# Kernel optimization log

Hardware: AMD Instinct MI355X
Metric: run time of the kernel (lower is better)

## Reference

```python
import jax, jax.numpy as jnp
import numpy as np
from jax import lax

QK_K = 256          # elements per Q6_K super-block
TYPE_SIZE = 210     # bytes per Q6_K super-block (128 ql + 64 qh + 16 scales + 2 d)
OUT_F = 14336
IN_F = 4096


def setup_inputs() -> dict:
    key = jax.random.key(0)
    kx, kb = jax.random.split(key)
    x = jax.random.normal(kx, (16, 1, IN_F), dtype=jnp.float32)
    bias = jax.random.normal(kb, (OUT_F,), dtype=jnp.float32) * 0.02

    # Build realistic packed Q6_K weight bytes with numpy (bit packing).
    rng = np.random.default_rng(0)
    n_blocks = OUT_F * IN_F // QK_K
    ql = rng.integers(0, 256, (n_blocks, 128), dtype=np.uint8)
    qh = rng.integers(0, 256, (n_blocks, 64), dtype=np.uint8)
    scales = rng.integers(-32, 32, (n_blocks, 16)).astype(np.int8).view(np.uint8)
    d = (rng.standard_normal(n_blocks) * 0.004).astype(np.float16).view(np.uint8).reshape(n_blocks, 2)
    w_q = jnp.asarray(np.concatenate([ql, qh, scales, d], axis=1))  # [n_blocks, 210] uint8
    return {"x": x, "w_q": w_q, "bias": bias}


def _dequant_q6_k(w_q, out_f, in_f):
    # w_q: [n_blocks, 210] uint8 -> [out_f, in_f] float32
    n = w_q.shape[0]
    ql = w_q[:, :128].astype(jnp.int32)
    qh = w_q[:, 128:192].astype(jnp.int32)
    sc = lax.bitcast_convert_type(w_q[:, 192:208], jnp.int8).astype(jnp.float32)  # [n,16]
    d_u16 = w_q[:, 208].astype(jnp.uint16) | (w_q[:, 209].astype(jnp.uint16) << 8)
    d = lax.bitcast_convert_type(d_u16, jnp.float16).astype(jnp.float32)          # [n]
    dl = (d[:, None] * sc).reshape(n, 16, 1)                                      # per-16-elt scale

    shift_l = jnp.array([0, 4], dtype=jnp.int32).reshape(1, 1, 2, 1)
    ql = ((ql.reshape(n, 2, 1, 64) >> shift_l) & 15).reshape(n, 8, 32)
    shift_h = jnp.array([0, 2, 4, 6], dtype=jnp.int32).reshape(1, 1, 4, 1)
    qh = ((qh.reshape(n, 2, 1, 32) >> shift_h) & 3).reshape(n, 8, 32)
    q = (ql | (qh << 4)) - 32                                                     # int in [-32, 31]
    w = dl * q.reshape(n, 16, 16).astype(jnp.float32)
    return w.reshape(out_f, in_f)


def reference(x, w_q, bias):
    in_f = x.shape[-1]
    out_f = bias.shape[0]
    w = _dequant_q6_k(w_q, out_f, in_f)          # [out_f, in_f]
    return jnp.einsum("bsi,oi->bso", x, w) + bias
```

## Files before the change

kernel.cpp:

```cpp
#include <hip/hip_runtime.h>
#include <hip/hip_bf16.h>
#include <hip/hip_fp16.h>
#include <stdint.h>


#define OUT_F 14336
#define IN_F  4096
#define NB    16

using f32x4  = __attribute__((ext_vector_type(4))) float;
using short8 = __attribute__((ext_vector_type(8))) short;

constexpr int ROWS = 64;
constexpr int SBS  = 2;
constexpr int SLOT = 216;
constexpr int ROWSTRIDE = SBS * SLOT + 8;
constexpr int KSPLIT = IN_F / (SBS * 256);

__device__ __forceinline__ float ub(uint32_t v, int i) {
  return (float)((v >> (8 * i)) & 0xffu);
}
__device__ __forceinline__ uint32_t pack_bf16(float lo, float hi) {
  return (__builtin_bit_cast(uint32_t, lo) >> 16) |
         (__builtin_bit_cast(uint32_t, hi) & 0xffff0000u);
}

__global__ __launch_bounds__(256)
void prep_kernel(const float* __restrict__ x, const float* __restrict__ bias,
                 float* __restrict__ out, ushort* __restrict__ xbf, int use_ws)
{
  const int t = blockIdx.x * 256 + threadIdx.x;
  if (t < NB * OUT_F) {
    out[t] = bias[t % OUT_F];
  }
  if (use_ws && t < NB * IN_F) {
    uint32_t u = __builtin_bit_cast(uint32_t, x[t]);
    xbf[t] = (ushort)((u + 0x8000u) >> 16);
  }
}

template<bool USE_WS>
__global__ __launch_bounds__(256, 4)
void q6k_gemm(const int* __restrict__ wq,
              const float* __restrict__ xf,
              const ushort* __restrict__ xbf,
              float* __restrict__ out)
{
  __shared__ uint8_t lds[ROWS * ROWSTRIDE];
  const int tid = threadIdx.x;
  const int bx  = blockIdx.x;
  const int by  = blockIdx.y;
  const int row_base = bx * ROWS;

  ushort* lds16 = (ushort*)lds;
  for (int i = tid; i < ROWS * 105; i += 256) {
    const int r = i / 105;
    const int d = i - r * 105;
    const int4 q4 = *(const int4*)(wq + (size_t)(row_base + r) * 3360 + by * 420 + 4 * d);
    const uint32_t v = (uint32_t)(q4.x & 0xff) | ((uint32_t)(q4.y & 0xff) << 8) |
                       ((uint32_t)(q4.z & 0xff) << 16) | ((uint32_t)q4.w << 24);
    const int b0 = 4 * d, b1 = 4 * d + 2;
    const int sb0 = b0 / 210, sb1 = b1 / 210;
    lds16[(r * ROWSTRIDE + sb0 * SLOT + (b0 - sb0 * 210)) >> 1] = (ushort)v;
    lds16[(r * ROWSTRIDE + sb1 * SLOT + (b1 - sb1 * 210)) >> 1] = (ushort)(v >> 16);
  }
  __syncthreads();

  const int lane = tid & 63;
  const int wv   = tid >> 6;
  const int l15  = lane & 15;
  const int lg   = lane >> 4;
  const int sc_sh = 8 * (lane >> 5);

  f32x4 acc = {0.f, 0.f, 0.f, 0.f};
  const int k_blk = by * (SBS * 256);
  const uint8_t* rowslot = lds + (wv * 16 + l15) * ROWSTRIDE;

  #pragma unroll
  for (int sb = 0; sb < SBS; ++sb) {
    const uint8_t* slot = rowslot + sb * SLOT;
    const uint2 sc01 = *(const uint2*)(slot + 192);
    const uint2 sc23 = *(const uint2*)(slot + 200);
    const float dsup = __half2float(*(const __half*)(slot + 208));
    const int k_sb = k_blk + sb * 256 + 8 * lg;

    #pragma unroll
    for (int m = 0; m < 8; ++m) {
      const uint2 ql = *(const uint2*)(slot + (m >> 2) * 64 + (m & 1) * 32 + 8 * lg);
      const uint2 qh = *(const uint2*)(slot + 128 + (m >> 2) * 32 + 8 * lg);

      const uint32_t scw = (m >> 1) == 0 ? sc01.x : (m >> 1) == 1 ? sc01.y
                         : (m >> 1) == 2 ? sc23.x : sc23.y;
      const int sc = (int)(int8_t)(scw >> (16 * (m & 1) + sc_sh));
      const float dl  = dsup * (float)sc;
      const float mdl = -32.0f * dl;

      const int SL = 4 * ((m >> 1) & 1);
      const int SH = 2 * (m & 3);
      const uint32_t t0 = (ql.x >> SL) & 0x0F0F0F0Fu;
      const uint32_t t1 = (ql.y >> SL) & 0x0F0F0F0Fu;
      const uint32_t h0 = (qh.x >> SH) & 0x03030303u;
      const uint32_t h1 = (qh.y >> SH) & 0x03030303u;
      const uint32_t q0 = t0 | (h0 << 4);
      const uint32_t q1 = t1 | (h1 << 4);

      const float w0 = fmaf(ub(q0, 0), dl, mdl);
      const float w1 = fmaf(ub(q0, 1), dl, mdl);
      const float w2 = fmaf(ub(q0, 2), dl, mdl);
      const float w3 = fmaf(ub(q0, 3), dl, mdl);
      const float w4 = fmaf(ub(q1, 0), dl, mdl);
      const float w5 = fmaf(ub(q1, 1), dl, mdl);
      const float w6 = fmaf(ub(q1, 2), dl, mdl);
      const float w7 = fmaf(ub(q1, 3), dl, mdl);

      union { short8 s; uint32_t u[4]; } bfr;
      bfr.u[0] = pack_bf16(w0, w1);
      bfr.u[1] = pack_bf16(w2, w3);
      bfr.u[2] = pack_bf16(w4, w5);
      bfr.u[3] = pack_bf16(w6, w7);

      short8 afrag;
      if constexpr (USE_WS) {
        afrag = *(const short8*)(xbf + (size_t)l15 * IN_F + k_sb + m * 32);
      } else {
        const float* xp = xf + (size_t)l15 * IN_F + k_sb + m * 32;
        const f32x4 v0 = *(const f32x4*)(xp);
        const f32x4 v1 = *(const f32x4*)(xp + 4);
        union { short8 s; uint32_t u[4]; } av;
        av.u[0] = pack_bf16(v0[0], v0[1]);
        av.u[1] = pack_bf16(v0[2], v0[3]);
        av.u[2] = pack_bf16(v1[0], v1[1]);
        av.u[3] = pack_bf16(v1[2], v1[3]);
        afrag = av.s;
      }

      acc = __builtin_amdgcn_mfma_f32_16x16x32_bf16(afrag, bfr.s, acc, 0, 0, 0);
    }
  }

  const int o = row_base + wv * 16 + l15;
  #pragma unroll
  for (int r = 0; r < 4; ++r) {
    atomicAdd(&out[(size_t)(lg * 4 + r) * OUT_F + o], acc[r]);
  }
}

extern "C" void kernel_launch(void* const* d_in, const int* in_sizes, int n_in,
                              void* d_out, int out_size, void* d_ws, size_t ws_size,
                              hipStream_t stream)
{
  const float* x    = (const float*)d_in[0];
  const int*   wq   = (const int*)d_in[1];
  const float* bias = (const float*)d_in[2];
  float*  out = (float*)d_out;
  ushort* xbf = (ushort*)d_ws;
  const bool use_ws = ws_size >= (size_t)NB * IN_F * 2;

  prep_kernel<<<dim3((NB * OUT_F + 255) / 256), dim3(256), 0, stream>>>(
      x, bias, out, xbf, use_ws ? 1 : 0);

  dim3 grid(OUT_F / ROWS, KSPLIT);
  if (use_ws) {
    q6k_gemm<true><<<grid, dim3(256), 0, stream>>>(wq, x, xbf, out);
  } else {
    q6k_gemm<false><<<grid, dim3(256), 0, stream>>>(wq, x, xbf, out);
  }
}
```

Before: 52.85 us.

## Read Q6_K weight bytes directly from global memory, drop LDS staging

Removes the shared-memory staging pass and block barrier. Each lane now loads its weight bytes straight from global memory, where the weight tensor is stored as one int per byte, and dequantizes them in registers. This cuts the LDS write/read traffic and the __syncthreads. In exchange each lane issues many small strided 8-byte global loads per MFMA step instead of coalesced 16-byte loads, which may hurt memory coalescing and cache efficiency.

Result: slower. 55.87 us (+5.7%).

```diff
diff --git a/kernel.cpp b/kernel.cpp
--- a/kernel.cpp
+++ b/kernel.cpp
@@ -11,15 +11,9 @@
 using f32x4  = __attribute__((ext_vector_type(4))) float;
 using short8 = __attribute__((ext_vector_type(8))) short;
 
-constexpr int ROWS = 64;
-constexpr int SBS  = 2;
-constexpr int SLOT = 216;
-constexpr int ROWSTRIDE = SBS * SLOT + 8;
-constexpr int KSPLIT = IN_F / (SBS * 256);
+constexpr int ROWS   = 64;
+constexpr int KSPLIT = 8;
 
-__device__ __forceinline__ float ub(uint32_t v, int i) {
-  return (float)((v >> (8 * i)) & 0xffu);
-}
 __device__ __forceinline__ uint32_t pack_bf16(float lo, float hi) {
   return (__builtin_bit_cast(uint32_t, lo) >> 16) |
          (__builtin_bit_cast(uint32_t, hi) & 0xffff0000u);
@@ -46,78 +40,58 @@
               const ushort* __restrict__ xbf,
               float* __restrict__ out)
 {
-  __shared__ uint8_t lds[ROWS * ROWSTRIDE];
-  const int tid = threadIdx.x;
-  const int bx  = blockIdx.x;
-  const int by  = blockIdx.y;
-  const int row_base = bx * ROWS;
-
-  ushort* lds16 = (ushort*)lds;
-  for (int i = tid; i < ROWS * 105; i += 256) {
-    const int r = i / 105;
-    const int d = i - r * 105;
-    const int4 q4 = *(const int4*)(wq + (size_t)(row_base + r) * 3360 + by * 420 + 4 * d);
-    const uint32_t v = (uint32_t)(q4.x & 0xff) | ((uint32_t)(q4.y & 0xff) << 8) |
-                       ((uint32_t)(q4.z & 0xff) << 16) | ((uint32_t)q4.w << 24);
-    const int b0 = 4 * d, b1 = 4 * d + 2;
-    const int sb0 = b0 / 210, sb1 = b1 / 210;
-    lds16[(r * ROWSTRIDE + sb0 * SLOT + (b0 - sb0 * 210)) >> 1] = (ushort)v;
-    lds16[(r * ROWSTRIDE + sb1 * SLOT + (b1 - sb1 * 210)) >> 1] = (ushort)(v >> 16);
-  }
-  __syncthreads();
-
+  const int tid  = threadIdx.x;
   const int lane = tid & 63;
   const int wv   = tid >> 6;
   const int l15  = lane & 15;
   const int lg   = lane >> 4;
-  const int sc_sh = 8 * (lane >> 5);
+  const int hb   = lg >> 1;
+  const int by   = blockIdx.y;
+
+  const int row = blockIdx.x * ROWS + wv * 16 + l15;
+  const int* base = wq + (size_t)row * 3360 + by * 420;
+  const int k_blk = by * 512;
 
   f32x4 acc = {0.f, 0.f, 0.f, 0.f};
-  const int k_blk = by * (SBS * 256);
-  const uint8_t* rowslot = lds + (wv * 16 + l15) * ROWSTRIDE;
 
   #pragma unroll
-  for (int sb = 0; sb < SBS; ++sb) {
-    const uint8_t* slot = rowslot + sb * SLOT;
-    const uint2 sc01 = *(const uint2*)(slot + 192);
-    const uint2 sc23 = *(const uint2*)(slot + 200);
-    const float dsup = __half2float(*(const __half*)(slot + 208));
+  for (int sb = 0; sb < 2; ++sb) {
+    const int* sbase = base + sb * 210;
+    const uint2 dd = *(const uint2*)(sbase + 208);
+    const float dsup = __half2float(
+        __builtin_bit_cast(__half, (uint16_t)((dd.x & 0xffu) | ((dd.y & 0xffu) << 8))));
     const int k_sb = k_blk + sb * 256 + 8 * lg;
 
     #pragma unroll
     for (int m = 0; m < 8; ++m) {
-      const uint2 ql = *(const uint2*)(slot + (m >> 2) * 64 + (m & 1) * 32 + 8 * lg);
-      const uint2 qh = *(const uint2*)(slot + 128 + (m >> 2) * 32 + 8 * lg);
+      const int* qlp = sbase + (m >> 2) * 64 + (m & 1) * 32 + 8 * lg;
+      const int* qhp = sbase + 128 + (m >> 2) * 32 + 8 * lg;
+      const uint2 a0 = *(const uint2*)(qlp);
+      const uint2 a1 = *(const uint2*)(qlp + 2);
+      const uint2 a2 = *(const uint2*)(qlp + 4);
+      const uint2 a3 = *(const uint2*)(qlp + 6);
+      const uint2 b0 = *(const uint2*)(qhp);
+      const uint2 b1 = *(const uint2*)(qhp + 2);
+      const uint2 b2 = *(const uint2*)(qhp + 4);
+      const uint2 b3 = *(const uint2*)(qhp + 6);
+      const uint2 scp = *(const uint2*)(sbase + 192 + 2 * m);
 
-      const uint32_t scw = (m >> 1) == 0 ? sc01.x : (m >> 1) == 1 ? sc01.y
-                         : (m >> 1) == 2 ? sc23.x : sc23.y;
-      const int sc = (int)(int8_t)(scw >> (16 * (m & 1) + sc_sh));
+      const int sc = (int)(int8_t)(uint8_t)(hb ? scp.y : scp.x);
       const float dl  = dsup * (float)sc;
       const float mdl = -32.0f * dl;
 
       const int SL = 4 * ((m >> 1) & 1);
       const int SH = 2 * (m & 3);
-      const uint32_t t0 = (ql.x >> SL) & 0x0F0F0F0Fu;
-      const uint32_t t1 = (ql.y >> SL) & 0x0F0F0F0Fu;
-      const uint32_t h0 = (qh.x >> SH) & 0x03030303u;
-      const uint32_t h1 = (qh.y >> SH) & 0x03030303u;
-      const uint32_t q0 = t0 | (h0 << 4);
-      const uint32_t q1 = t1 | (h1 << 4);
-
-      const float w0 = fmaf(ub(q0, 0), dl, mdl);
-      const float w1 = fmaf(ub(q0, 1), dl, mdl);
-      const float w2 = fmaf(ub(q0, 2), dl, mdl);
-      const float w3 = fmaf(ub(q0, 3), dl, mdl);
-      const float w4 = fmaf(ub(q1, 0), dl, mdl);
-      const float w5 = fmaf(ub(q1, 1), dl, mdl);
-      const float w6 = fmaf(ub(q1, 2), dl, mdl);
-      const float w7 = fmaf(ub(q1, 3), dl, mdl);
+      auto dq = [&](uint32_t q, uint32_t h) -> float {
+        const uint32_t t = ((q >> SL) & 15u) | (((h >> SH) & 3u) << 4);
+        return fmaf((float)t, dl, mdl);
+      };
 
       union { short8 s; uint32_t u[4]; } bfr;
-      bfr.u[0] = pack_bf16(w0, w1);
-      bfr.u[1] = pack_bf16(w2, w3);
-      bfr.u[2] = pack_bf16(w4, w5);
-      bfr.u[3] = pack_bf16(w6, w7);
+      bfr.u[0] = pack_bf16(dq(a0.x, b0.x), dq(a0.y, b0.y));
+      bfr.u[1] = pack_bf16(dq(a1.x, b1.x), dq(a1.y, b1.y));
+      bfr.u[2] = pack_bf16(dq(a2.x, b2.x), dq(a2.y, b2.y));
+      bfr.u[3] = pack_bf16(dq(a3.x, b3.x), dq(a3.y, b3.y));
 
       short8 afrag;
       if constexpr (USE_WS) {
@@ -138,10 +112,9 @@
     }
   }
 
-  const int o = row_base + wv * 16 + l15;
   #pragma unroll
   for (int r = 0; r < 4; ++r) {
-    atomicAdd(&out[(size_t)(lg * 4 + r) * OUT_F + o], acc[r]);
+    atomicAdd(&out[(size_t)(lg * 4 + r) * OUT_F + row], acc[r]);
   }
 }
 
```
